# Kernel optimization log

Hardware: AMD Instinct MI355X
Metric: run time of the kernel (lower is better)

The kernel has to match this reference:

```python
import jax, jax.numpy as jnp
import numpy as np

EMBED = 1024
HEADS = 16
HEAD_DIM = EMBED // HEADS


def setup_inputs() -> dict:
    key = jax.random.key(0)
    ks = jax.random.split(key, 6)
    N, S = 2, 2048
    scale = 1.0 / np.sqrt(EMBED)
    x = jax.random.normal(ks[0], (N, S, EMBED), dtype=jnp.float32)
    # nn.Linear weights are [out, in]; y = x @ W.T
    Wq = jax.random.normal(ks[1], (EMBED, EMBED), dtype=jnp.float32) * scale
    Wk = jax.random.normal(ks[2], (EMBED, EMBED), dtype=jnp.float32) * scale
    Wv = jax.random.normal(ks[3], (EMBED, EMBED), dtype=jnp.float32) * scale
    Wo = jax.random.normal(ks[4], (EMBED, EMBED), dtype=jnp.float32) * scale
    bo = jax.random.normal(ks[5], (EMBED,), dtype=jnp.float32) * 0.01
    return {"x": x, "Wq": Wq, "Wk": Wk, "Wv": Wv, "Wo": Wo, "bo": bo}


def reference(x, Wq, Wk, Wv, Wo, bo):
    N, S, E = x.shape
    # projections (torch Linear: x @ W.T)
    def split_heads(t):
        return t.reshape(N, S, HEADS, HEAD_DIM).transpose(0, 2, 1, 3)  # [N,H,S,D]
    q = split_heads(x @ Wq.T)
    k = split_heads(x @ Wk.T)
    v = split_heads(x @ Wv.T)
    # scores scaled by sqrt(embed_size), faithful to original
    scores = jnp.einsum('nhqd,nhkd->nhqk', q, k) / jnp.sqrt(jnp.float32(E))
    attn = jax.nn.softmax(scores, axis=-1)
    out = jnp.einsum('nhqk,nhkd->nhqd', attn, v)  # [N,H,S,D]
    out = out.transpose(0, 2, 1, 3).reshape(N, S, E)
    return out @ Wo.T + bo
```

## Files before the change

### kernel.cpp

```cpp
#include <hip/hip_runtime.h>

#define E   1024
#define SQ  2048
#define NR  4096

typedef _Float16 half8 __attribute__((ext_vector_type(8)));
typedef _Float16 half4 __attribute__((ext_vector_type(4)));
typedef float    f32x4 __attribute__((ext_vector_type(4)));

#define MFMA_F16(a, b, c) __builtin_amdgcn_mfma_f32_16x16x32_f16((a), (b), (c), 0, 0, 0)

__device__ __forceinline__ void async16(const void* g, void* l) {
  __builtin_amdgcn_global_load_lds((const __attribute__((address_space(1))) void*)g,
                                   (__attribute__((address_space(3))) void*)l, 16, 0, 0);
}

__device__ __forceinline__ float bperm_f(int srclane, float v) {
  return __int_as_float(__builtin_amdgcn_ds_bpermute(srclane << 2, __float_as_int(v)));
}

__global__ __launch_bounds__(256)
void cvtall(const float* __restrict__ x, const float* __restrict__ wq,
            const float* __restrict__ wk, const float* __restrict__ wv,
            const float* __restrict__ wo,
            _Float16* __restrict__ xh, _Float16* __restrict__ wqh,
            _Float16* __restrict__ wkh, _Float16* __restrict__ wvh,
            _Float16* __restrict__ woh) {
  int b = blockIdx.x;
  const float* src; _Float16* dst; int off;
  if (b < 4096)      { src = x;  dst = xh;  off = b; }
  else if (b < 5120) { src = wq; dst = wqh; off = b - 4096; }
  else if (b < 6144) { src = wk; dst = wkh; off = b - 5120; }
  else if (b < 7168) { src = wv; dst = wvh; off = b - 6144; }
  else               { src = wo; dst = woh; off = b - 7168; }
  int i = off * 256 + threadIdx.x;
  f32x4 v = ((const f32x4*)src)[i];
  ((half4*)dst)[i] = __builtin_convertvector(v, half4);
}

template <bool OUTF32>
__global__ __launch_bounds__(256, 2)
void gemm_bt(const _Float16* __restrict__ A,
             const _Float16* __restrict__ B0, const _Float16* __restrict__ B1,
             const _Float16* __restrict__ B2,
             _Float16* __restrict__ C0, _Float16* __restrict__ C1,
             _Float16* __restrict__ C2,
             float* __restrict__ Cf, const float* __restrict__ bias,
             int M, int N, int K)
{
  const int z = blockIdx.z;
  const _Float16* B = (z == 0) ? B0 : ((z == 1) ? B1 : B2);
  _Float16* C = (z == 0) ? C0 : ((z == 1) ? C1 : C2);
  __shared__ _Float16 As[128 * 64];
  __shared__ _Float16 Bs[128 * 64];
  const int tid = threadIdx.x;
  const int w = tid >> 6, lane = tid & 63;
  const int lr = lane & 15, lg = lane >> 4;
  const int l8 = lane >> 3, l7 = lane & 7;
  const int gch = l7 ^ (l8 & 7);
  const int tm = blockIdx.x * 128, tn = blockIdx.y * 128;
  const int wr = w >> 1, wc = w & 1;
  const int sl7 = lr & 7;

  const f32x4 zv = {0.f, 0.f, 0.f, 0.f};
  f32x4 acc[4][4];
  #pragma unroll
  for (int mi = 0; mi < 4; mi++)
    #pragma unroll
    for (int ni = 0; ni < 4; ni++) acc[mi][ni] = zv;

  for (int ks = 0; ks < K; ks += 64) {
    #pragma unroll
    for (int ci = 0; ci < 4; ci++) {
      int c = w + ci * 4;
      async16(A + (size_t)(tm + c * 8 + l8) * K + ks + gch * 8, (void*)(As + c * 512));
    }
    #pragma unroll
    for (int ci = 0; ci < 4; ci++) {
      int c = w + ci * 4;
      async16(B + (size_t)(tn + c * 8 + l8) * K + ks + gch * 8, (void*)(Bs + c * 512));
    }
    __syncthreads();
    #pragma unroll
    for (int kk = 0; kk < 2; kk++) {
      const int sl = ((kk * 4 + lg) ^ sl7) << 4;
      half8 af[4], bf[4];
      #pragma unroll
      for (int mi = 0; mi < 4; mi++)
        af[mi] = *(const half8*)((const char*)As + (wr * 64 + mi * 16 + lr) * 128 + sl);
      #pragma unroll
      for (int ni = 0; ni < 4; ni++)
        bf[ni] = *(const half8*)((const char*)Bs + (wc * 64 + ni * 16 + lr) * 128 + sl);
      #pragma unroll
      for (int mi = 0; mi < 4; mi++)
        #pragma unroll
        for (int ni = 0; ni < 4; ni++)
          acc[mi][ni] = MFMA_F16(af[mi], bf[ni], acc[mi][ni]);
    }
    __syncthreads();
  }
  #pragma unroll
  for (int mi = 0; mi < 4; mi++) {
    const int row = tm + wr * 64 + mi * 16 + 4 * lg;
    #pragma unroll
    for (int ni = 0; ni < 4; ni++) {
      const int col = tn + wc * 64 + ni * 16 + lr;
      #pragma unroll
      for (int j = 0; j < 4; j++) {
        if constexpr (OUTF32)
          Cf[(size_t)(row + j) * N + col] = acc[mi][ni][j] + bias[col];
        else
          C[(size_t)(row + j) * N + col] = (_Float16)acc[mi][ni][j];
      }
    }
  }
}

__global__ __launch_bounds__(256)
void vtrans(const _Float16* __restrict__ V, _Float16* __restrict__ Vg2) {
  __shared__ _Float16 Vl[64][72];
  const int tid = threadIdx.x;
  const int s0 = blockIdx.x * 64;
  const int nb = blockIdx.y;
  const _Float16* src = V + (size_t)(nb >> 4) * SQ * E + (size_t)s0 * E + (nb & 15) * 64;
  #pragma unroll
  for (int i = 0; i < 2; i++) {
    int c = tid + 256 * i; int s = c >> 3, d0 = (c & 7) * 8;
    *(half8*)(&Vl[s][d0]) = *(const half8*)(src + (size_t)s * E + d0);
  }
  __syncthreads();
  #pragma unroll
  for (int i = 0; i < 2; i++) {
    int c = tid + 256 * i; int d = c >> 3, m = c & 7;
    half8 o;
    #pragma unroll
    for (int r = 0; r < 8; r++) {
      int p = 8 * m + r;
      int kv = (p & 32) | (((p >> 2) & 1) << 4) | (((p >> 3) & 3) << 2) | (p & 3);
      o[r] = Vl[kv][d];
    }
    *(half8*)(Vg2 + ((size_t)nb * 64 + d) * SQ + s0 + 8 * m) = o;
  }
}

__global__ __launch_bounds__(256, 2)
void attn_kernel(const _Float16* __restrict__ Q, const _Float16* __restrict__ Kg,
                 const _Float16* __restrict__ Vg2, _Float16* __restrict__ Og)
{
  __shared__ _Float16 Ks[2][64 * 64];
  __shared__ _Float16 Vt[2][64 * 64];
  const int tid = threadIdx.x;
  const int w = tid >> 6, lane = tid & 63;
  const int lr = lane & 15, lg = lane >> 4;
  const int l8 = lane >> 3, l7 = lane & 7;
  const int nb = blockIdx.y;
  const size_t hb  = (size_t)(nb >> 4) * SQ * E + (size_t)(nb & 15) * 64;
  const size_t hb2 = (size_t)nb * 64 * SQ;
  const int qbase = blockIdx.x * 128 + w * 32;
  const int gsl = (l7 ^ (l8 & 7)) * 8;
  const int sl7 = lr & 7;

  half8 qf[2][2];
  #pragma unroll
  for (int qi = 0; qi < 2; qi++)
    #pragma unroll
    for (int kd = 0; kd < 2; kd++) {
      half8 v = *(const half8*)(Q + hb + (size_t)(qbase + qi * 16 + lr) * E + kd * 32 + lg * 8);
      qf[qi][kd] = v * (_Float16)0.03125f;
    }

  const f32x4 zv = {0.f, 0.f, 0.f, 0.f};
  f32x4 o[2][4];
  float ms[2] = {-1e30f, -1e30f}, ls[2] = {0.f, 0.f};
  #pragma unroll
  for (int mi = 0; mi < 2; mi++)
    #pragma unroll
    for (int nd = 0; nd < 4; nd++) o[mi][nd] = zv;

  #pragma unroll
  for (int ci = 0; ci < 2; ci++) {
    int c = w + ci * 4;
    async16(Kg  + hb  + (size_t)(c * 8 + l8) * E  + gsl, (void*)(Ks[0] + c * 512));
    async16(Vg2 + hb2 + (size_t)(c * 8 + l8) * SQ + gsl, (void*)(Vt[0] + c * 512));
  }
  __syncthreads();

  int cur = 0;
  for (int t = 0; t < 32; t++) {
    if (t < 31) {
      const int kvb = (t + 1) * 64;
      #pragma unroll
      for (int ci = 0; ci < 2; ci++) {
        int c = w + ci * 4;
        async16(Kg  + hb  + (size_t)(kvb + c * 8 + l8) * E + gsl, (void*)(Ks[cur ^ 1] + c * 512));
        async16(Vg2 + hb2 + (size_t)(c * 8 + l8) * SQ + kvb + gsl, (void*)(Vt[cur ^ 1] + c * 512));
      }
    }
    f32x4 s[2][4];
    #pragma unroll
    for (int qi = 0; qi < 2; qi++)
      #pragma unroll
      for (int ni = 0; ni < 4; ni++) s[qi][ni] = zv;
    #pragma unroll
    for (int kd = 0; kd < 2; kd++) {
      const int sl = ((kd * 4 + lg) ^ sl7) << 4;
      half8 kf[4];
      #pragma unroll
      for (int ni = 0; ni < 4; ni++)
        kf[ni] = *(const half8*)((const char*)Ks[cur] + (ni * 16 + lr) * 128 + sl);
      #pragma unroll
      for (int qi = 0; qi < 2; qi++)
        #pragma unroll
        for (int ni = 0; ni < 4; ni++)
          s[qi][ni] = MFMA_F16(kf[ni], qf[qi][kd], s[qi][ni]);
    }
    float corr[2];
    #pragma unroll
    for (int qi = 0; qi < 2; qi++) {
      float m0 = fmaxf(fmaxf(s[qi][0][0], s[qi][0][1]), fmaxf(s[qi][0][2], s[qi][0][3]));
      float m1 = fmaxf(fmaxf(s[qi][1][0], s[qi][1][1]), fmaxf(s[qi][1][2], s[qi][1][3]));
      float m2 = fmaxf(fmaxf(s[qi][2][0], s[qi][2][1]), fmaxf(s[qi][2][2], s[qi][2][3]));
      float m3 = fmaxf(fmaxf(s[qi][3][0], s[qi][3][1]), fmaxf(s[qi][3][2], s[qi][3][3]));
      float mx = fmaxf(fmaxf(m0, m1), fmaxf(m2, m3));
      mx = fmaxf(mx, __shfl_xor(mx, 16));
      mx = fmaxf(mx, __shfl_xor(mx, 32));
      float mnew = fmaxf(ms[qi], mx);
      float c = __expf(ms[qi] - mnew);
      corr[qi] = c;
      float rs = 0.f;
      #pragma unroll
      for (int ni = 0; ni < 4; ni++)
        #pragma unroll
        for (int jr = 0; jr < 4; jr++) {
          float p = __expf(s[qi][ni][jr] - mnew);
          s[qi][ni][jr] = p;
          rs += p;
        }
      rs += __shfl_xor(rs, 16);
      rs += __shfl_xor(rs, 32);
      ls[qi] = ls[qi] * c + rs;
      ms[qi] = mnew;
    }
    #pragma unroll
    for (int mi = 0; mi < 2; mi++)
      #pragma unroll
      for (int jr = 0; jr < 4; jr++) {
        float c4 = bperm_f(4 * lg + jr, corr[mi]);
        #pragma unroll
        for (int nd = 0; nd < 4; nd++) o[mi][nd][jr] *= c4;
      }
    half8 pa[2][2];
    #pragma unroll
    for (int mi = 0; mi < 2; mi++)
      #pragma unroll
      for (int kk = 0; kk < 2; kk++)
        #pragma unroll
        for (int j2 = 0; j2 < 8; j2++)
          pa[mi][kk][j2] = (_Float16)s[mi][2 * kk + (j2 >> 2)][j2 & 3];
    #pragma unroll
    for (int kk = 0; kk < 2; kk++) {
      const int sl = ((kk * 4 + lg) ^ sl7) << 4;
      half8 vf[4];
      #pragma unroll
      for (int nd = 0; nd < 4; nd++)
        vf[nd] = *(const half8*)((const char*)Vt[cur] + (nd * 16 + lr) * 128 + sl);
      #pragma unroll
      for (int mi = 0; mi < 2; mi++)
        #pragma unroll
        for (int nd = 0; nd < 4; nd++)
          o[mi][nd] = MFMA_F16(pa[mi][kk], vf[nd], o[mi][nd]);
    }
    __syncthreads();
    cur ^= 1;
  }
  #pragma unroll
  for (int mi = 0; mi < 2; mi++) {
    float li = 1.0f / ls[mi];
    #pragma unroll
    for (int jr = 0; jr < 4; jr++) {
      float lv = bperm_f(4 * lg + jr, li);
      const int row = qbase + mi * 16 + 4 * lg + jr;
      #pragma unroll
      for (int nd = 0; nd < 4; nd++)
        Og[hb + (size_t)row * E + nd * 16 + lr] = (_Float16)(o[mi][nd][jr] * lv);
    }
  }
}

extern "C" void kernel_launch(void* const* d_in, const int* in_sizes, int n_in,
                              void* d_out, int out_size, void* d_ws, size_t ws_size,
                              hipStream_t stream)
{
  const float* x  = (const float*)d_in[0];
  const float* Wq = (const float*)d_in[1];
  const float* Wk = (const float*)d_in[2];
  const float* Wv = (const float*)d_in[3];
  const float* Wo = (const float*)d_in[4];
  const float* bo = (const float*)d_in[5];
  char* ws = (char*)d_ws;
  const size_t MB = 1024u * 1024u;
  _Float16* xh  = (_Float16*)(ws);
  _Float16* Vg2 = (_Float16*)(ws);
  _Float16* Wqh = (_Float16*)(ws + 8 * MB);
  _Float16* Wkh = (_Float16*)(ws + 10 * MB);
  _Float16* Wvh = (_Float16*)(ws + 12 * MB);
  _Float16* Woh = (_Float16*)(ws + 14 * MB);
  _Float16* Vh  = (_Float16*)(ws + 16 * MB);
  _Float16* Oh  = (_Float16*)(ws + 24 * MB);
  _Float16* Qh  = (_Float16*)(d_out);
  _Float16* Kh  = (_Float16*)((char*)d_out + 8 * MB);
  float* Y = (float*)d_out;

  cvtall<<<8192, 256, 0, stream>>>(x, Wq, Wk, Wv, Wo, xh, Wqh, Wkh, Wvh, Woh);

  gemm_bt<false><<<dim3(32, 8, 3), 256, 0, stream>>>(
      xh, Wqh, Wkh, Wvh, Qh, Kh, Vh, nullptr, nullptr, NR, E, E);

  vtrans<<<dim3(32, 32), 256, 0, stream>>>(Vh, Vg2);

  attn_kernel<<<dim3(16, 32), 256, 0, stream>>>(Qh, Kh, Vg2, Oh);

  gemm_bt<true><<<dim3(32, 8, 1), 256, 0, stream>>>(
      Oh, Woh, Woh, Woh, nullptr, nullptr, nullptr, Y, bo, NR, E, E);
}
```

Before: 203.0 us.

## Fuse V transpose into QKV GEMM, exp2 softmax with lazy rescale, smaller attention tiles

The separate V transpose kernel is removed. The QKV GEMM epilogue now writes V directly in the permuted transposed layout, and Q is stored pre-scaled by log2(e)/32. The attention kernel now handles 16 query rows per wave with 64-row blocks, a swizzled block order and occupancy 4. It uses exp2, skips the rescale whenever the running max grows by at most 8, and packs probabilities with cvt_pkrtz. The output projection uses 64-row tiles to launch more blocks. These changes trade larger per-wave K/V reuse and exact max tracking for more parallelism and fewer kernels, and the skipped rescale relies on fp32 headroom.

```diff
diff --git a/kernel.cpp b/kernel.cpp
--- a/kernel.cpp
+++ b/kernel.cpp
@@ -4,11 +4,20 @@
 #define SQ  2048
 #define NR  4096
 
-typedef _Float16 half8 __attribute__((ext_vector_type(8)));
-typedef _Float16 half4 __attribute__((ext_vector_type(4)));
-typedef float    f32x4 __attribute__((ext_vector_type(4)));
+typedef _Float16 half8  __attribute__((ext_vector_type(8)));
+typedef _Float16 half4  __attribute__((ext_vector_type(4)));
+typedef __fp16   fp16x2 __attribute__((ext_vector_type(2)));
+typedef float    f32x4  __attribute__((ext_vector_type(4)));
 
 #define MFMA_F16(a, b, c) __builtin_amdgcn_mfma_f32_16x16x32_f16((a), (b), (c), 0, 0, 0)
+
+#if __has_builtin(__builtin_amdgcn_exp2f)
+#define EXP2(x) __builtin_amdgcn_exp2f(x)
+#else
+#define EXP2(x) exp2f(x)
+#endif
+
+#define QSCALE 0.04508422002778011f
 
 __device__ __forceinline__ void async16(const void* g, void* l) {
   __builtin_amdgcn_global_load_lds((const __attribute__((address_space(1))) void*)g,
@@ -38,19 +47,16 @@
   ((half4*)dst)[i] = __builtin_convertvector(v, half4);
 }
 
-template <bool OUTF32>
 __global__ __launch_bounds__(256, 2)
-void gemm_bt(const _Float16* __restrict__ A,
-             const _Float16* __restrict__ B0, const _Float16* __restrict__ B1,
-             const _Float16* __restrict__ B2,
-             _Float16* __restrict__ C0, _Float16* __restrict__ C1,
-             _Float16* __restrict__ C2,
-             float* __restrict__ Cf, const float* __restrict__ bias,
-             int M, int N, int K)
+void gemm_qkv(const _Float16* __restrict__ A,
+              const _Float16* __restrict__ B0, const _Float16* __restrict__ B1,
+              const _Float16* __restrict__ B2,
+              _Float16* __restrict__ C0, _Float16* __restrict__ C1,
+              _Float16* __restrict__ Vg2,
+              int M, int N, int K)
 {
   const int z = blockIdx.z;
   const _Float16* B = (z == 0) ? B0 : ((z == 1) ? B1 : B2);
-  _Float16* C = (z == 0) ? C0 : ((z == 1) ? C1 : C2);
   __shared__ _Float16 As[128 * 64];
   __shared__ _Float16 Bs[128 * 64];
   const int tid = threadIdx.x;
@@ -99,51 +105,105 @@
     }
     __syncthreads();
   }
-  #pragma unroll
-  for (int mi = 0; mi < 4; mi++) {
-    const int row = tm + wr * 64 + mi * 16 + 4 * lg;
+  if (z == 2) {
+    #pragma unroll
+    for (int mi = 0; mi < 4; mi++) {
+      const int row = tm + wr * 64 + mi * 16 + 4 * lg;
+      const int n = row >> 11;
+      const int s0 = (row & 2047) & ~63;
+      const int cb = 32 * (mi >> 1) + 8 * lg + 4 * (mi & 1);
+      #pragma unroll
+      for (int ni = 0; ni < 4; ni++) {
+        const int d = tn + wc * 64 + ni * 16 + lr;
+        const int nb = n * 16 + (d >> 6);
+        half4 hv = __builtin_convertvector(acc[mi][ni], half4);
+        *(half4*)(Vg2 + ((size_t)nb * 64 + (d & 63)) * SQ + s0 + cb) = hv;
+      }
+    }
+  } else {
+    _Float16* C = (z == 0) ? C0 : C1;
+    const float sc = (z == 0) ? QSCALE : 1.0f;
+    #pragma unroll
+    for (int mi = 0; mi < 4; mi++) {
+      const int row = tm + wr * 64 + mi * 16 + 4 * lg;
+      #pragma unroll
+      for (int ni = 0; ni < 4; ni++) {
+        const int col = tn + wc * 64 + ni * 16 + lr;
+        #pragma unroll
+        for (int j = 0; j < 4; j++)
+          C[(size_t)(row + j) * N + col] = (_Float16)(acc[mi][ni][j] * sc);
+      }
+    }
+  }
+}
+
+__global__ __launch_bounds__(256, 2)
+void gemm_o(const _Float16* __restrict__ A, const _Float16* __restrict__ B,
+            float* __restrict__ Cf, const float* __restrict__ bias,
+            int M, int N, int K)
+{
+  __shared__ _Float16 As[64 * 64];
+  __shared__ _Float16 Bs[128 * 64];
+  const int tid = threadIdx.x;
+  const int w = tid >> 6, lane = tid & 63;
+  const int lr = lane & 15, lg = lane >> 4;
+  const int l8 = lane >> 3, l7 = lane & 7;
+  const int gch = l7 ^ (l8 & 7);
+  const int tm = blockIdx.x * 64, tn = blockIdx.y * 128;
+  const int wr = w >> 1, wc = w & 1;
+  const int sl7 = lr & 7;
+
+  const f32x4 zv = {0.f, 0.f, 0.f, 0.f};
+  f32x4 acc[2][4];
+  #pragma unroll
+  for (int mi = 0; mi < 2; mi++)
+    #pragma unroll
+    for (int ni = 0; ni < 4; ni++) acc[mi][ni] = zv;
+
+  for (int ks = 0; ks < K; ks += 64) {
+    #pragma unroll
+    for (int ci = 0; ci < 2; ci++) {
+      int c = w + ci * 4;
+      async16(A + (size_t)(tm + c * 8 + l8) * K + ks + gch * 8, (void*)(As + c * 512));
+    }
+    #pragma unroll
+    for (int ci = 0; ci < 4; ci++) {
+      int c = w + ci * 4;
+      async16(B + (size_t)(tn + c * 8 + l8) * K + ks + gch * 8, (void*)(Bs + c * 512));
+    }
+    __syncthreads();
+    #pragma unroll
+    for (int kk = 0; kk < 2; kk++) {
+      const int sl = ((kk * 4 + lg) ^ sl7) << 4;
+      half8 af[2], bf[4];
+      #pragma unroll
+      for (int mi = 0; mi < 2; mi++)
+        af[mi] = *(const half8*)((const char*)As + (wr * 32 + mi * 16 + lr) * 128 + sl);
+      #pragma unroll
+      for (int ni = 0; ni < 4; ni++)
+        bf[ni] = *(const half8*)((const char*)Bs + (wc * 64 + ni * 16 + lr) * 128 + sl);
+      #pragma unroll
+      for (int mi = 0; mi < 2; mi++)
+        #pragma unroll
+        for (int ni = 0; ni < 4; ni++)
+          acc[mi][ni] = MFMA_F16(af[mi], bf[ni], acc[mi][ni]);
+    }
+    __syncthreads();
+  }
+  #pragma unroll
+  for (int mi = 0; mi < 2; mi++) {
+    const int row = tm + wr * 32 + mi * 16 + 4 * lg;
     #pragma unroll
     for (int ni = 0; ni < 4; ni++) {
       const int col = tn + wc * 64 + ni * 16 + lr;
       #pragma unroll
-      for (int j = 0; j < 4; j++) {
-        if constexpr (OUTF32)
-          Cf[(size_t)(row + j) * N + col] = acc[mi][ni][j] + bias[col];
-        else
-          C[(size_t)(row + j) * N + col] = (_Float16)acc[mi][ni][j];
-      }
-    }
-  }
-}
-
-__global__ __launch_bounds__(256)
-void vtrans(const _Float16* __restrict__ V, _Float16* __restrict__ Vg2) {
-  __shared__ _Float16 Vl[64][72];
-  const int tid = threadIdx.x;
-  const int s0 = blockIdx.x * 64;
-  const int nb = blockIdx.y;
-  const _Float16* src = V + (size_t)(nb >> 4) * SQ * E + (size_t)s0 * E + (nb & 15) * 64;
-  #pragma unroll
-  for (int i = 0; i < 2; i++) {
-    int c = tid + 256 * i; int s = c >> 3, d0 = (c & 7) * 8;
-    *(half8*)(&Vl[s][d0]) = *(const half8*)(src + (size_t)s * E + d0);
-  }
-  __syncthreads();
-  #pragma unroll
-  for (int i = 0; i < 2; i++) {
-    int c = tid + 256 * i; int d = c >> 3, m = c & 7;
-    half8 o;
-    #pragma unroll
-    for (int r = 0; r < 8; r++) {
-      int p = 8 * m + r;
-      int kv = (p & 32) | (((p >> 2) & 1) << 4) | (((p >> 3) & 3) << 2) | (p & 3);
-      o[r] = Vl[kv][d];
-    }
-    *(half8*)(Vg2 + ((size_t)nb * 64 + d) * SQ + s0 + 8 * m) = o;
-  }
-}
-
-__global__ __launch_bounds__(256, 2)
+      for (int j = 0; j < 4; j++)
+        Cf[(size_t)(row + j) * N + col] = acc[mi][ni][j] + bias[col];
+    }
+  }
+}
+
+__global__ __launch_bounds__(256, 4)
 void attn_kernel(const _Float16* __restrict__ Q, const _Float16* __restrict__ Kg,
                  const _Float16* __restrict__ Vg2, _Float16* __restrict__ Og)
 {
@@ -153,29 +213,25 @@
   const int w = tid >> 6, lane = tid & 63;
   const int lr = lane & 15, lg = lane >> 4;
   const int l8 = lane >> 3, l7 = lane & 7;
-  const int nb = blockIdx.y;
+  const int id = blockIdx.x + 32 * blockIdx.y;
+  const int wid = (id & 7) * 128 + (id >> 3);
+  const int qb = wid & 31, nb = wid >> 5;
   const size_t hb  = (size_t)(nb >> 4) * SQ * E + (size_t)(nb & 15) * 64;
   const size_t hb2 = (size_t)nb * 64 * SQ;
-  const int qbase = blockIdx.x * 128 + w * 32;
+  const int qbase = qb * 64 + w * 16;
   const int gsl = (l7 ^ (l8 & 7)) * 8;
   const int sl7 = lr & 7;
 
-  half8 qf[2][2];
-  #pragma unroll
-  for (int qi = 0; qi < 2; qi++)
-    #pragma unroll
-    for (int kd = 0; kd < 2; kd++) {
-      half8 v = *(const half8*)(Q + hb + (size_t)(qbase + qi * 16 + lr) * E + kd * 32 + lg * 8);
-      qf[qi][kd] = v * (_Float16)0.03125f;
-    }
+  half8 qf[2];
+  #pragma unroll
+  for (int kd = 0; kd < 2; kd++)
+    qf[kd] = *(const half8*)(Q + hb + (size_t)(qbase + lr) * E + kd * 32 + lg * 8);
 
   const f32x4 zv = {0.f, 0.f, 0.f, 0.f};
-  f32x4 o[2][4];
-  float ms[2] = {-1e30f, -1e30f}, ls[2] = {0.f, 0.f};
-  #pragma unroll
-  for (int mi = 0; mi < 2; mi++)
-    #pragma unroll
-    for (int nd = 0; nd < 4; nd++) o[mi][nd] = zv;
+  f32x4 o[4];
+  float ms = -1e30f, ls = 0.f;
+  #pragma unroll
+  for (int nd = 0; nd < 4; nd++) o[nd] = zv;
 
   #pragma unroll
   for (int ci = 0; ci < 2; ci++) {
@@ -196,11 +252,9 @@
         async16(Vg2 + hb2 + (size_t)(c * 8 + l8) * SQ + kvb + gsl, (void*)(Vt[cur ^ 1] + c * 512));
       }
     }
-    f32x4 s[2][4];
-    #pragma unroll
-    for (int qi = 0; qi < 2; qi++)
-      #pragma unroll
-      for (int ni = 0; ni < 4; ni++) s[qi][ni] = zv;
+    f32x4 s[4];
+    #pragma unroll
+    for (int ni = 0; ni < 4; ni++) s[ni] = zv;
     #pragma unroll
     for (int kd = 0; kd < 2; kd++) {
       const int sl = ((kd * 4 + lg) ^ sl7) << 4;
@@ -209,54 +263,62 @@
       for (int ni = 0; ni < 4; ni++)
         kf[ni] = *(const half8*)((const char*)Ks[cur] + (ni * 16 + lr) * 128 + sl);
       #pragma unroll
-      for (int qi = 0; qi < 2; qi++)
-        #pragma unroll
-        for (int ni = 0; ni < 4; ni++)
-          s[qi][ni] = MFMA_F16(kf[ni], qf[qi][kd], s[qi][ni]);
-    }
-    float corr[2];
-    #pragma unroll
-    for (int qi = 0; qi < 2; qi++) {
-      float m0 = fmaxf(fmaxf(s[qi][0][0], s[qi][0][1]), fmaxf(s[qi][0][2], s[qi][0][3]));
-      float m1 = fmaxf(fmaxf(s[qi][1][0], s[qi][1][1]), fmaxf(s[qi][1][2], s[qi][1][3]));
-      float m2 = fmaxf(fmaxf(s[qi][2][0], s[qi][2][1]), fmaxf(s[qi][2][2], s[qi][2][3]));
-      float m3 = fmaxf(fmaxf(s[qi][3][0], s[qi][3][1]), fmaxf(s[qi][3][2], s[qi][3][3]));
+      for (int ni = 0; ni < 4; ni++)
+        s[ni] = MFMA_F16(kf[ni], qf[kd], s[ni]);
+    }
+    {
+      float m0 = fmaxf(fmaxf(s[0][0], s[0][1]), fmaxf(s[0][2], s[0][3]));
+      float m1 = fmaxf(fmaxf(s[1][0], s[1][1]), fmaxf(s[1][2], s[1][3]));
+      float m2 = fmaxf(fmaxf(s[2][0], s[2][1]), fmaxf(s[2][2], s[2][3]));
+      float m3 = fmaxf(fmaxf(s[3][0], s[3][1]), fmaxf(s[3][2], s[3][3]));
       float mx = fmaxf(fmaxf(m0, m1), fmaxf(m2, m3));
       mx = fmaxf(mx, __shfl_xor(mx, 16));
       mx = fmaxf(mx, __shfl_xor(mx, 32));
-      float mnew = fmaxf(ms[qi], mx);
-      float c = __expf(ms[qi] - mnew);
-      corr[qi] = c;
-      float rs = 0.f;
-      #pragma unroll
-      for (int ni = 0; ni < 4; ni++)
+      if (__all(mx <= ms + 8.0f)) {
+        float rs = 0.f;
+        #pragma unroll
+        for (int ni = 0; ni < 4; ni++)
+          #pragma unroll
+          for (int jr = 0; jr < 4; jr++) {
+            float p = EXP2(s[ni][jr] - ms);
+            s[ni][jr] = p; rs += p;
+          }
+        rs += __shfl_xor(rs, 16);
+        rs += __shfl_xor(rs, 32);
+        ls += rs;
+      } else {
+        float mnew = fmaxf(ms, mx);
+        float corr = EXP2(ms - mnew);
+        ms = mnew;
+        float rs = 0.f;
+        #pragma unroll
+        for (int ni = 0; ni < 4; ni++)
+          #pragma unroll
+          for (int jr = 0; jr < 4; jr++) {
+            float p = EXP2(s[ni][jr] - ms);
+            s[ni][jr] = p; rs += p;
+          }
+        rs += __shfl_xor(rs, 16);
+        rs += __shfl_xor(rs, 32);
+        ls = ls * corr + rs;
         #pragma unroll
         for (int jr = 0; jr < 4; jr++) {
-          float p = __expf(s[qi][ni][jr] - mnew);
-          s[qi][ni][jr] = p;
-          rs += p;
+          float c4 = bperm_f(4 * lg + jr, corr);
+          #pragma unroll
+          for (int nd = 0; nd < 4; nd++) o[nd][jr] *= c4;
         }
-      rs += __shfl_xor(rs, 16);
-      rs += __shfl_xor(rs, 32);
-      ls[qi] = ls[qi] * c + rs;
-      ms[qi] = mnew;
-    }
-    #pragma unroll
-    for (int mi = 0; mi < 2; mi++)
-      #pragma unroll
-      for (int jr = 0; jr < 4; jr++) {
-        float c4 = bperm_f(4 * lg + jr, corr[mi]);
-        #pragma unroll
-        for (int nd = 0; nd < 4; nd++) o[mi][nd][jr] *= c4;
       }
-    half8 pa[2][2];
-    #pragma unroll
-    for (int mi = 0; mi < 2; mi++)
-      #pragma unroll
-      for (int kk = 0; kk < 2; kk++)
-        #pragma unroll
-        for (int j2 = 0; j2 < 8; j2++)
-          pa[mi][kk][j2] = (_Float16)s[mi][2 * kk + (j2 >> 2)][j2 & 3];
+    }
+    half8 pa[2];
+    #pragma unroll
+    for (int kk = 0; kk < 2; kk++) {
+      union { half8 h8; fp16x2 h2[4]; } u;
+      u.h2[0] = __builtin_amdgcn_cvt_pkrtz(s[2 * kk][0], s[2 * kk][1]);
+      u.h2[1] = __builtin_amdgcn_cvt_pkrtz(s[2 * kk][2], s[2 * kk][3]);
+      u.h2[2] = __builtin_amdgcn_cvt_pkrtz(s[2 * kk + 1][0], s[2 * kk + 1][1]);
+      u.h2[3] = __builtin_amdgcn_cvt_pkrtz(s[2 * kk + 1][2], s[2 * kk + 1][3]);
+      pa[kk] = u.h8;
+    }
     #pragma unroll
     for (int kk = 0; kk < 2; kk++) {
       const int sl = ((kk * 4 + lg) ^ sl7) << 4;
@@ -265,24 +327,21 @@
       for (int nd = 0; nd < 4; nd++)
         vf[nd] = *(const half8*)((const char*)Vt[cur] + (nd * 16 + lr) * 128 + sl);
       #pragma unroll
-      for (int mi = 0; mi < 2; mi++)
-        #pragma unroll
-        for (int nd = 0; nd < 4; nd++)
-          o[mi][nd] = MFMA_F16(pa[mi][kk], vf[nd], o[mi][nd]);
+      for (int nd = 0; nd < 4; nd++)
+        o[nd] = MFMA_F16(pa[kk], vf[nd], o[nd]);
     }
     __syncthreads();
     cur ^= 1;
   }
-  #pragma unroll
-  for (int mi = 0; mi < 2; mi++) {
-    float li = 1.0f / ls[mi];
+  {
+    float li = 1.0f / ls;
     #pragma unroll
     for (int jr = 0; jr < 4; jr++) {
       float lv = bperm_f(4 * lg + jr, li);
-      const int row = qbase + mi * 16 + 4 * lg + jr;
+      const int row = qbase + 4 * lg + jr;
       #pragma unroll
       for (int nd = 0; nd < 4; nd++)
-        Og[hb + (size_t)row * E + nd * 16 + lr] = (_Float16)(o[mi][nd][jr] * lv);
+        Og[hb + (size_t)row * E + nd * 16 + lr] = (_Float16)(o[nd][jr] * lv);
     }
   }
 }
@@ -300,12 +359,11 @@
   char* ws = (char*)d_ws;
   const size_t MB = 1024u * 1024u;
   _Float16* xh  = (_Float16*)(ws);
-  _Float16* Vg2 = (_Float16*)(ws);
   _Float16* Wqh = (_Float16*)(ws + 8 * MB);
   _Float16* Wkh = (_Float16*)(ws + 10 * MB);
   _Float16* Wvh = (_Float16*)(ws + 12 * MB);
   _Float16* Woh = (_Float16*)(ws + 14 * MB);
-  _Float16* Vh  = (_Float16*)(ws + 16 * MB);
+  _Float16* Vg2 = (_Float16*)(ws + 16 * MB);
   _Float16* Oh  = (_Float16*)(ws + 24 * MB);
   _Float16* Qh  = (_Float16*)(d_out);
   _Float16* Kh  = (_Float16*)((char*)d_out + 8 * MB);
@@ -313,13 +371,10 @@
 
   cvtall<<<8192, 256, 0, stream>>>(x, Wq, Wk, Wv, Wo, xh, Wqh, Wkh, Wvh, Woh);
 
-  gemm_bt<false><<<dim3(32, 8, 3), 256, 0, stream>>>(
-      xh, Wqh, Wkh, Wvh, Qh, Kh, Vh, nullptr, nullptr, NR, E, E);
-
-  vtrans<<<dim3(32, 32), 256, 0, stream>>>(Vh, Vg2);
-
-  attn_kernel<<<dim3(16, 32), 256, 0, stream>>>(Qh, Kh, Vg2, Oh);
-
-  gemm_bt<true><<<dim3(32, 8, 1), 256, 0, stream>>>(
-      Oh, Woh, Woh, Woh, nullptr, nullptr, nullptr, Y, bo, NR, E, E);
-}
+  gemm_qkv<<<dim3(32, 8, 3), 256, 0, stream>>>(
+      xh, Wqh, Wkh, Wvh, Qh, Kh, Vg2, NR, E, E);
+
+  attn_kernel<<<dim3(32, 32), 256, 0, stream>>>(Qh, Kh, Vg2, Oh);
+
+  gemm_o<<<dim3(64, 8), 256, 0, stream>>>(Oh, Woh, Y, bo, NR, E, E);
+}
```

Result: faster. 186.7 us (-8.0%).
